# Kernel tuning notes

Measured on AMD Instinct MI355X. Metric: run time of the kernel, lower is better.

Reference implementation:

```python
import jax, jax.numpy as jnp
import numpy as np

B, T, HID = 4, 2048, 1024
H, D = 16, 64  # num_heads, depth = hidden // heads
NEG_INF = -1e9


def setup_inputs() -> dict:
    key = jax.random.key(0)
    ks = jax.random.split(key, 8)
    s = 1.0 / np.sqrt(HID)
    return {
        "q": jax.random.normal(ks[0], (B, T, HID), jnp.float32),
        "k": jax.random.normal(ks[1], (B, T, HID), jnp.float32),
        "v": jax.random.normal(ks[2], (B, T, HID), jnp.float32),
        "pad_mask": jax.random.randint(ks[3], (B, T), 0, 2, jnp.int32),
        "Wq": jax.random.normal(ks[4], (HID, HID), jnp.float32) * s,
        "Wk": jax.random.normal(ks[5], (HID, HID), jnp.float32) * s,
        "Wv": jax.random.normal(ks[6], (HID, HID), jnp.float32) * s,
        "Wo": jax.random.normal(ks[7], (HID, HID), jnp.float32) * s,
    }


def _split_heads(x):
    # [B, T, HID] -> [B*H, T, D]
    b, t, _ = x.shape
    return x.reshape(b, t, H, D).transpose(0, 2, 1, 3).reshape(b * H, t, D)


def _combine_heads(x):
    # [B*H, T, D] -> [B, T, HID]
    t = x.shape[1]
    return x.reshape(-1, H, t, D).transpose(0, 2, 1, 3).reshape(-1, t, HID)


def reference(q, k, v, pad_mask, Wq, Wk, Wv, Wo):
    qp = _split_heads(q @ Wq) * (D ** -0.5)   # [B*H, Tq, D]
    kp = _split_heads(k @ Wk)                  # [B*H, Tk, D]
    vp = _split_heads(v @ Wv)                  # [B*H, Tk, D]
    # additive pad bias: repeat([H,1]) is head-major tiling, reproduced via jnp.tile
    bias = jnp.tile(pad_mask.astype(jnp.float32) * NEG_INF, (H, 1))[:, None, :]
    logits = jnp.einsum('bqd,bkd->bqk', qp, kp) + bias  # [B*H, Tq, Tk]
    weights = jax.nn.softmax(logits, axis=-1)
    # original calls functional.dropout but discards the result -> no-op
    out = jnp.einsum('bqk,bkd->bqd', weights, vp)
    out = _combine_heads(out)                  # [B, Tq, HID]
    return out @ Wo
```

## Files before the change

kernel.cpp:

```cpp
#include <hip/hip_runtime.h>
#include <hip/hip_bf16.h>

#define TQ 2048
#define HIDDEN 1024
#define NB 4
#define NH 16
#define DH 64
#define BHN (NB*NH)
#define LOG2E 1.44269504f

typedef __attribute__((ext_vector_type(4))) float f32x4;
typedef __attribute__((ext_vector_type(8))) short s16x8;

#if __has_builtin(__builtin_amdgcn_exp2f)
#define EXP2(x) __builtin_amdgcn_exp2f(x)
#else
#define EXP2(x) exp2f(x)
#endif

__device__ inline unsigned short f2bf(float f) {
    union { float f; unsigned int u; } x; x.f = f;
    unsigned int r = x.u + 0x7fffu + ((x.u >> 16) & 1u);
    return (unsigned short)(r >> 16);
}

__device__ inline unsigned int pkbf(float a, float b) {
    __hip_bfloat162 h = __float22bfloat162_rn(make_float2(a, b));
    return *reinterpret_cast<unsigned int*>(&h);
}

union PBU { uint4 u4; s16x8 v; };

#define GLL16(gsrc, ldst) \
    __builtin_amdgcn_global_load_lds( \
        (const __attribute__((address_space(1))) unsigned int*)(gsrc), \
        (__attribute__((address_space(3))) unsigned int*)(ldst), 16, 0, 0)

__global__ __launch_bounds__(256) void maskprep(const int* __restrict__ pad,
                                                unsigned short* __restrict__ maskAndB) {
    int p = blockIdx.x * 256 + threadIdx.x;
    int r = p >> 11, off = p & 2047;
    int o6 = off & 63;
    int ks = o6 >> 5, k32 = o6 & 31;
    int lg = k32 >> 3, j = k32 & 7;
    int key = (off & ~63) | (ks * 32 + ((j >> 2) << 4) + (lg << 2) + (j & 3));
    maskAndB[p] = pad[r * 2048 + key] ? (unsigned short)0 : (unsigned short)0xFFFF;
}

__global__ __launch_bounds__(256) void wt_kernel(const float* W0, const float* W1,
                                                 const float* W2, const float* W3,
                                                 unsigned short* Wt) {
    const float* W = (blockIdx.z == 0) ? W0 : (blockIdx.z == 1) ? W1
                    : (blockIdx.z == 2) ? W2 : W3;
    unsigned short* out = Wt + (size_t)blockIdx.z * HIDDEN * HIDDEN;
    __shared__ float tile[64][68];
    int t = threadIdx.x;
    int k0 = blockIdx.y * 64, n0 = blockIdx.x * 64;
#pragma unroll
    for (int i = 0; i < 4; i++) {
        int r = (t >> 4) + i * 16;
        int c = (t & 15) * 4;
        float4 v = *(const float4*)(W + (size_t)(k0 + r) * HIDDEN + n0 + c);
        tile[r][c] = v.x; tile[r][c+1] = v.y; tile[r][c+2] = v.z; tile[r][c+3] = v.w;
    }
    __syncthreads();
#pragma unroll
    for (int i = 0; i < 4; i++) {
        int n = (t >> 4) + i * 16;
        int kc = (t & 15) * 4;
        ushort4 o;
        o.x = f2bf(tile[kc+0][n]); o.y = f2bf(tile[kc+1][n]);
        o.z = f2bf(tile[kc+2][n]); o.w = f2bf(tile[kc+3][n]);
        *(ushort4*)(out + (size_t)(n0 + n) * HIDDEN + k0 + kc) = o;
    }
}

__global__ __launch_bounds__(256) void gemm_proj(const float* __restrict__ A,
                                                 const unsigned short* __restrict__ Bt,
                                                 unsigned short* __restrict__ outb,
                                                 float scale, int vt) {
    __shared__ alignas(16) float As[128 * 64];
    __shared__ alignas(16) unsigned short Bs[128 * 64];
    const int t = threadIdx.x;
    const int wave = t >> 6, lane = t & 63;
    const int wr = wave >> 1, wc = wave & 1;
    const int lr = lane & 15, lg = lane >> 4;
    const int linear = blockIdx.x + 8 * blockIdx.y;
    const int tile = ((linear & 7) << 6) | (linear >> 3);
    const int m0 = (tile >> 3) * 128, n0 = (tile & 7) * 128;

    size_t gA[8];
#pragma unroll
    for (int i = 0; i < 8; i++) {
        int f = i * 256 + t;
        int row = f >> 4, sg = (f & 15) ^ (row & 15);
        gA[i] = (size_t)(m0 + row) * HIDDEN + sg * 4;
    }
    size_t gB[4];
#pragma unroll
    for (int i = 0; i < 4; i++) {
        int f = i * 256 + t;
        int row = f >> 3, sg = (f & 7) ^ (row & 7);
        gB[i] = (size_t)(n0 + row) * HIDDEN + sg * 8;
    }

    f32x4 acc[4][4] = {};

    for (int k0 = 0; k0 < HIDDEN; k0 += 64) {
        __syncthreads();
#pragma unroll
        for (int i = 0; i < 8; i++)
            GLL16(A + gA[i] + k0, &As[(size_t)(i * 256 + wave * 64) * 4]);
#pragma unroll
        for (int i = 0; i < 4; i++)
            GLL16(Bt + gB[i] + k0, &Bs[(size_t)(i * 256 + wave * 64) * 8]);
        __syncthreads();
#pragma unroll
        for (int q = 0; q < 2; q++) {
            s16x8 af[4], bfr[4];
#pragma unroll
            for (int mi = 0; mi < 4; mi++) {
                int row = wr * 64 + mi * 16 + lr;
                int s0 = (q * 8 + lg * 2) ^ (row & 15);
                int s1 = (q * 8 + lg * 2 + 1) ^ (row & 15);
                float4 a0 = *(const float4*)(&As[row * 64 + s0 * 4]);
                float4 a1 = *(const float4*)(&As[row * 64 + s1 * 4]);
                PBU u;
                u.u4.x = pkbf(a0.x, a0.y); u.u4.y = pkbf(a0.z, a0.w);
                u.u4.z = pkbf(a1.x, a1.y); u.u4.w = pkbf(a1.z, a1.w);
                af[mi] = u.v;
            }
#pragma unroll
            for (int ni = 0; ni < 4; ni++) {
                int row = wc * 64 + ni * 16 + lr;
                int s = (q * 4 + lg) ^ (row & 7);
                bfr[ni] = *(const s16x8*)(&Bs[row * 64 + s * 8]);
            }
#pragma unroll
            for (int mi = 0; mi < 4; mi++)
#pragma unroll
                for (int ni = 0; ni < 4; ni++)
                    acc[mi][ni] = __builtin_amdgcn_mfma_f32_16x16x32_bf16(af[mi], bfr[ni], acc[mi][ni], 0, 0, 0);
        }
    }

    if (vt == 0) {
#pragma unroll
        for (int mi = 0; mi < 4; mi++)
#pragma unroll
            for (int ni = 0; ni < 4; ni++)
#pragma unroll
                for (int j = 0; j < 4; j++) {
                    int m = m0 + wr * 64 + mi * 16 + lg * 4 + j;
                    int n = n0 + wc * 64 + ni * 16 + lr;
                    int b = m >> 11, tt = m & (TQ - 1);
                    int h = n >> 6, d = n & 63;
                    outb[((size_t)(b * NH + h) * TQ + tt) * DH + d] = f2bf(acc[mi][ni][j] * scale);
                }
    } else {
#pragma unroll
        for (int mi = 0; mi < 4; mi++)
#pragma unroll
            for (int ni = 0; ni < 4; ni++) {
                int m = m0 + wr * 64 + mi * 16 + lg * 4;
                int n = n0 + wc * 64 + ni * 16 + lr;
                int b = m >> 11, tt = m & (TQ - 1);
                int h = n >> 6, d = n & 63;
                ushort4 pk;
                pk.x = f2bf(acc[mi][ni][0] * scale);
                pk.y = f2bf(acc[mi][ni][1] * scale);
                pk.z = f2bf(acc[mi][ni][2] * scale);
                pk.w = f2bf(acc[mi][ni][3] * scale);
                *(ushort4*)(outb + ((size_t)(b * NH + h) * DH + d) * TQ + tt) = pk;
            }
    }
}

__global__ __launch_bounds__(256) void gemm_out(const unsigned short* __restrict__ A,
                                                const unsigned short* __restrict__ Bt,
                                                float* __restrict__ out) {
    __shared__ alignas(16) unsigned short As[128 * 64];
    __shared__ alignas(16) unsigned short Bs[128 * 64];
    const int t = threadIdx.x;
    const int wave = t >> 6, lane = t & 63;
    const int wr = wave >> 1, wc = wave & 1;
    const int lr = lane & 15, lg = lane >> 4;
    const int linear = blockIdx.x + 8 * blockIdx.y;
    const int tile = ((linear & 7) << 6) | (linear >> 3);
    const int m0 = (tile >> 3) * 128, n0 = (tile & 7) * 128;

    size_t gA[4], gB[4];
#pragma unroll
    for (int i = 0; i < 4; i++) {
        int f = i * 256 + t;
        int row = f >> 3, sg = (f & 7) ^ (row & 7);
        gA[i] = (size_t)(m0 + row) * HIDDEN + sg * 8;
        gB[i] = (size_t)(n0 + row) * HIDDEN + sg * 8;
    }

    f32x4 acc[4][4] = {};

    for (int k0 = 0; k0 < HIDDEN; k0 += 64) {
        __syncthreads();
#pragma unroll
        for (int i = 0; i < 4; i++) {
            GLL16(A + gA[i] + k0, &As[(size_t)(i * 256 + wave * 64) * 8]);
            GLL16(Bt + gB[i] + k0, &Bs[(size_t)(i * 256 + wave * 64) * 8]);
        }
        __syncthreads();
#pragma unroll
        for (int q = 0; q < 2; q++) {
            s16x8 af[4], bfr[4];
#pragma unroll
            for (int mi = 0; mi < 4; mi++) {
                int row = wr * 64 + mi * 16 + lr;
                int s = (q * 4 + lg) ^ (row & 7);
                af[mi] = *(const s16x8*)(&As[row * 64 + s * 8]);
            }
#pragma unroll
            for (int ni = 0; ni < 4; ni++) {
                int row = wc * 64 + ni * 16 + lr;
                int s = (q * 4 + lg) ^ (row & 7);
                bfr[ni] = *(const s16x8*)(&Bs[row * 64 + s * 8]);
            }
#pragma unroll
            for (int mi = 0; mi < 4; mi++)
#pragma unroll
                for (int ni = 0; ni < 4; ni++)
                    acc[mi][ni] = __builtin_amdgcn_mfma_f32_16x16x32_bf16(af[mi], bfr[ni], acc[mi][ni], 0, 0, 0);
        }
    }
#pragma unroll
    for (int mi = 0; mi < 4; mi++)
#pragma unroll
        for (int ni = 0; ni < 4; ni++)
#pragma unroll
            for (int j = 0; j < 4; j++) {
                int m = m0 + wr * 64 + mi * 16 + lg * 4 + j;
                int n = n0 + wc * 64 + ni * 16 + lr;
                out[(size_t)m * HIDDEN + n] = acc[mi][ni][j];
            }
}

__global__ __launch_bounds__(512, 4) void attn_kernel(
        const unsigned short* __restrict__ QP,
        const unsigned short* __restrict__ KP,
        const unsigned short* __restrict__ VT,
        const unsigned short* __restrict__ maskAndB,
        unsigned short* __restrict__ AO) {
    __shared__ alignas(16) unsigned short Ks[2][64 * 72];
    __shared__ alignas(16) unsigned short Vs[2][64 * 72];
    const int t = threadIdx.x, wave = t >> 6, lane = t & 63;
    const int lr = lane & 15, lg = lane >> 4;
    const int linear = blockIdx.x + 8 * blockIdx.y;
    const int bh = ((linear & 7) << 3) | ((linear >> 3) & 7);
    const int qb = linear >> 6;
    const int q0 = qb * 256 + wave * 32;
    const unsigned short* Qb = QP + (size_t)bh * TQ * DH;
    const unsigned short* Kb = KP + (size_t)bh * TQ * DH;
    const unsigned short* Vb = VT + (size_t)bh * DH * TQ;
    const unsigned short* mrow = maskAndB + (bh & (NB - 1)) * TQ;

    const short ob = (short)0x3F80;
    const s16x8 ones = {ob, ob, ob, ob, ob, ob, ob, ob};

    s16x8 qf[2][2];
#pragma unroll
    for (int u = 0; u < 2; u++)
#pragma unroll
        for (int h = 0; h < 2; h++)
            qf[u][h] = *(const s16x8*)(Qb + (size_t)(q0 + u * 16 + lr) * DH + h * 32 + lg * 8);

    const int srow = t >> 3, scol = (t & 7) * 8;
    const unsigned short* kA = Kb + srow * DH + scol;
    const unsigned short* vA = Vb + (size_t)srow * TQ + scol;
    const int ksO = srow * 72 + scol;
    const int cc = t & 7;
    const int vg = ((cc & 4) << 1) + ((cc & 1) << 2) + ((cc >> 1) & 1);
    const int vO = srow * 72 + vg * 4;

    uint4 kr, vr;
#define LOAD_TILE(kt_) do { \
        kr = *(const uint4*)(kA + (size_t)(kt_) * 4096); \
        vr = *(const uint4*)(vA + (size_t)(kt_) * 64); \
    } while (0)
#define STORE_TILE(b_) do { \
        *(uint4*)(&Ks[b_][ksO]) = kr; \
        *(uint2*)(&Vs[b_][vO])     = make_uint2(vr.x, vr.y); \
        *(uint2*)(&Vs[b_][vO + 8]) = make_uint2(vr.z, vr.w); \
    } while (0)

    f32x4 o[2][4] = {};
    f32x4 osum[2] = {};

    LOAD_TILE(0);
    STORE_TILE(0);

    const int NT = TQ / 64;
    for (int kt = 0; kt < NT; kt++) {
        __syncthreads();
        const int cur = kt & 1;
        if (kt + 1 < NT) LOAD_TILE(kt + 1);
        uint4 ma0 = *(const uint4*)(mrow + kt * 64 + lg * 8);
        uint4 ma1 = *(const uint4*)(mrow + kt * 64 + 32 + lg * 8);

        f32x4 z[2][4] = {};
#pragma unroll
        for (int ni = 0; ni < 4; ni++) {
            s16x8 kf0 = *(const s16x8*)(&Ks[cur][(ni * 16 + lr) * 72 + lg * 8]);
            s16x8 kf1 = *(const s16x8*)(&Ks[cur][(ni * 16 + lr) * 72 + 32 + lg * 8]);
#pragma unroll
            for (int u = 0; u < 2; u++) {
                z[u][ni] = __builtin_amdgcn_mfma_f32_16x16x32_bf16(kf0, qf[u][0], z[u][ni], 0, 0, 0);
                z[u][ni] = __builtin_amdgcn_mfma_f32_16x16x32_bf16(kf1, qf[u][1], z[u][ni], 0, 0, 0);
            }
        }

        PBU pb[2][2];
#pragma unroll
        for (int u = 0; u < 2; u++) {
#pragma unroll
            for (int ni = 0; ni < 4; ni++)
#pragma unroll
                for (int r = 0; r < 4; r++)
                    z[u][ni][r] = EXP2(z[u][ni][r]);
#pragma unroll
            for (int ks = 0; ks < 2; ks++) {
                pb[u][ks].u4.x = pkbf(z[u][2 * ks][0], z[u][2 * ks][1]);
                pb[u][ks].u4.y = pkbf(z[u][2 * ks][2], z[u][2 * ks][3]);
                pb[u][ks].u4.z = pkbf(z[u][2 * ks + 1][0], z[u][2 * ks + 1][1]);
                pb[u][ks].u4.w = pkbf(z[u][2 * ks + 1][2], z[u][2 * ks + 1][3]);
            }
            pb[u][0].u4.x &= ma0.x; pb[u][0].u4.y &= ma0.y;
            pb[u][0].u4.z &= ma0.z; pb[u][0].u4.w &= ma0.w;
            pb[u][1].u4.x &= ma1.x; pb[u][1].u4.y &= ma1.y;
            pb[u][1].u4.z &= ma1.z; pb[u][1].u4.w &= ma1.w;
        }

#pragma unroll
        for (int di = 0; di < 4; di++)
#pragma unroll
            for (int ks = 0; ks < 2; ks++) {
                s16x8 vf = *(const s16x8*)(&Vs[cur][(di * 16 + lr) * 72 + ks * 32 + lg * 8]);
#pragma unroll
                for (int u = 0; u < 2; u++)
                    o[u][di] = __builtin_amdgcn_mfma_f32_16x16x32_bf16(vf, pb[u][ks].v, o[u][di], 0, 0, 0);
            }
#pragma unroll
        for (int u = 0; u < 2; u++) {
            osum[u] = __builtin_amdgcn_mfma_f32_16x16x32_bf16(ones, pb[u][0].v, osum[u], 0, 0, 0);
            osum[u] = __builtin_amdgcn_mfma_f32_16x16x32_bf16(ones, pb[u][1].v, osum[u], 0, 0, 0);
        }

        if (kt + 1 < NT) STORE_TILE((kt + 1) & 1);
    }

    const int b = bh >> 4, h = bh & 15;
#pragma unroll
    for (int u = 0; u < 2; u++) {
        float inv = 1.f / osum[u][0];
        int tt = q0 + u * 16 + lr;
#pragma unroll
        for (int di = 0; di < 4; di++) {
            uint2 w;
            w.x = pkbf(o[u][di][0] * inv, o[u][di][1] * inv);
            w.y = pkbf(o[u][di][2] * inv, o[u][di][3] * inv);
            *(uint2*)(AO + (size_t)(b * TQ + tt) * HIDDEN + h * 64 + di * 16 + lg * 4) = w;
        }
    }
#undef LOAD_TILE
#undef STORE_TILE
}

extern "C" void kernel_launch(void* const* d_in, const int* in_sizes, int n_in,
                              void* d_out, int out_size, void* d_ws, size_t ws_size,
                              hipStream_t stream) {
    const float* q  = (const float*)d_in[0];
    const float* k  = (const float*)d_in[1];
    const float* v  = (const float*)d_in[2];
    const int* pad  = (const int*)d_in[3];
    const float* Wq = (const float*)d_in[4];
    const float* Wk = (const float*)d_in[5];
    const float* Wv = (const float*)d_in[6];
    const float* Wo = (const float*)d_in[7];
    float* out = (float*)d_out;

    unsigned short* ws = (unsigned short*)d_ws;
    unsigned short* Wt = ws;
    unsigned short* AO = ws + (size_t)4 * 1024 * 1024;
    unsigned short* QP = AO + (size_t)BHN * TQ * DH;
    unsigned short* KP = QP + (size_t)BHN * TQ * DH;
    unsigned short* VTb = KP + (size_t)BHN * TQ * DH;
    unsigned short* maskAndB = VTb + (size_t)BHN * TQ * DH;
    (void)ws_size; (void)in_sizes; (void)n_in; (void)out_size;

    dim3 b256(256);
    const dim3 gGemm(8, 64);
    maskprep<<<dim3(NB * TQ / 256), b256, 0, stream>>>(pad, maskAndB);
    wt_kernel<<<dim3(16, 16, 4), b256, 0, stream>>>(Wq, Wk, Wv, Wo, Wt);
    gemm_proj<<<gGemm, b256, 0, stream>>>(q, Wt + (size_t)0 * 1024 * 1024, QP, 0.125f * LOG2E, 0);
    gemm_proj<<<gGemm, b256, 0, stream>>>(k, Wt + (size_t)1 * 1024 * 1024, KP, 1.0f, 0);
    gemm_proj<<<gGemm, b256, 0, stream>>>(v, Wt + (size_t)2 * 1024 * 1024, VTb, 1.0f, 1);
    attn_kernel<<<dim3(8, 64), dim3(512), 0, stream>>>(QP, KP, VTb, maskAndB, AO);
    gemm_out<<<gGemm, b256, 0, stream>>>(AO, Wt + (size_t)3 * 1024 * 1024, out);
}
```

Before: 203.8 us.

## Use 1024-thread attention blocks with 16 query rows per wave

The attention kernel moves from 512 threads with 32 query rows per wave to 1024 threads with 16 rows per wave. The K/V tile loads are split so the first half of the threads loads K and the second half loads V. This is meant to raise wave-level parallelism and cut per-wave register use. In exchange, each K/V tile read from LDS is reused by fewer query rows per wave, so LDS traffic per MFMA rises, and the larger block raises barrier cost.

New measurement: 213.4 us. +4.7%, slower.

```diff
diff --git a/kernel.cpp b/kernel.cpp
--- a/kernel.cpp
+++ b/kernel.cpp
@@ -242,7 +242,7 @@
             }
 }
 
-__global__ __launch_bounds__(512, 4) void attn_kernel(
+__global__ __launch_bounds__(1024, 8) void attn_kernel(
         const unsigned short* __restrict__ QP,
         const unsigned short* __restrict__ KP,
         const unsigned short* __restrict__ VT,
@@ -255,7 +255,7 @@
     const int linear = blockIdx.x + 8 * blockIdx.y;
     const int bh = ((linear & 7) << 3) | ((linear >> 3) & 7);
     const int qb = linear >> 6;
-    const int q0 = qb * 256 + wave * 32;
+    const int q0 = qb * 256 + wave * 16;
     const unsigned short* Qb = QP + (size_t)bh * TQ * DH;
     const unsigned short* Kb = KP + (size_t)bh * TQ * DH;
     const unsigned short* Vb = VT + (size_t)bh * DH * TQ;
@@ -264,34 +264,35 @@
     const short ob = (short)0x3F80;
     const s16x8 ones = {ob, ob, ob, ob, ob, ob, ob, ob};
 
-    s16x8 qf[2][2];
-#pragma unroll
-    for (int u = 0; u < 2; u++)
-#pragma unroll
-        for (int h = 0; h < 2; h++)
-            qf[u][h] = *(const s16x8*)(Qb + (size_t)(q0 + u * 16 + lr) * DH + h * 32 + lg * 8);
-
-    const int srow = t >> 3, scol = (t & 7) * 8;
+    s16x8 qf0 = *(const s16x8*)(Qb + (size_t)(q0 + lr) * DH + lg * 8);
+    s16x8 qf1 = *(const s16x8*)(Qb + (size_t)(q0 + lr) * DH + 32 + lg * 8);
+
+    const int st = t & 511;
+    const int srow = st >> 3, scol = (st & 7) * 8;
+    const bool isK = t < 512;
     const unsigned short* kA = Kb + srow * DH + scol;
     const unsigned short* vA = Vb + (size_t)srow * TQ + scol;
     const int ksO = srow * 72 + scol;
-    const int cc = t & 7;
+    const int cc = st & 7;
     const int vg = ((cc & 4) << 1) + ((cc & 1) << 2) + ((cc >> 1) & 1);
     const int vO = srow * 72 + vg * 4;
 
-    uint4 kr, vr;
+    uint4 r;
 #define LOAD_TILE(kt_) do { \
-        kr = *(const uint4*)(kA + (size_t)(kt_) * 4096); \
-        vr = *(const uint4*)(vA + (size_t)(kt_) * 64); \
+        r = isK ? *(const uint4*)(kA + (size_t)(kt_) * 4096) \
+                : *(const uint4*)(vA + (size_t)(kt_) * 64); \
     } while (0)
 #define STORE_TILE(b_) do { \
-        *(uint4*)(&Ks[b_][ksO]) = kr; \
-        *(uint2*)(&Vs[b_][vO])     = make_uint2(vr.x, vr.y); \
-        *(uint2*)(&Vs[b_][vO + 8]) = make_uint2(vr.z, vr.w); \
+        if (isK) { \
+            *(uint4*)(&Ks[b_][ksO]) = r; \
+        } else { \
+            *(uint2*)(&Vs[b_][vO])     = make_uint2(r.x, r.y); \
+            *(uint2*)(&Vs[b_][vO + 8]) = make_uint2(r.z, r.w); \
+        } \
     } while (0)
 
-    f32x4 o[2][4] = {};
-    f32x4 osum[2] = {};
+    f32x4 o[4] = {};
+    f32x4 osum = {};
 
     LOAD_TILE(0);
     STORE_TILE(0);
@@ -304,69 +305,55 @@
         uint4 ma0 = *(const uint4*)(mrow + kt * 64 + lg * 8);
         uint4 ma1 = *(const uint4*)(mrow + kt * 64 + 32 + lg * 8);
 
-        f32x4 z[2][4] = {};
+        f32x4 z[4] = {};
 #pragma unroll
         for (int ni = 0; ni < 4; ni++) {
             s16x8 kf0 = *(const s16x8*)(&Ks[cur][(ni * 16 + lr) * 72 + lg * 8]);
             s16x8 kf1 = *(const s16x8*)(&Ks[cur][(ni * 16 + lr) * 72 + 32 + lg * 8]);
-#pragma unroll
-            for (int u = 0; u < 2; u++) {
-                z[u][ni] = __builtin_amdgcn_mfma_f32_16x16x32_bf16(kf0, qf[u][0], z[u][ni], 0, 0, 0);
-                z[u][ni] = __builtin_amdgcn_mfma_f32_16x16x32_bf16(kf1, qf[u][1], z[u][ni], 0, 0, 0);
-            }
-        }
-
-        PBU pb[2][2];
-#pragma unroll
-        for (int u = 0; u < 2; u++) {
-#pragma unroll
-            for (int ni = 0; ni < 4; ni++)
-#pragma unroll
-                for (int r = 0; r < 4; r++)
-                    z[u][ni][r] = EXP2(z[u][ni][r]);
-#pragma unroll
-            for (int ks = 0; ks < 2; ks++) {
-                pb[u][ks].u4.x = pkbf(z[u][2 * ks][0], z[u][2 * ks][1]);
-                pb[u][ks].u4.y = pkbf(z[u][2 * ks][2], z[u][2 * ks][3]);
-                pb[u][ks].u4.z = pkbf(z[u][2 * ks + 1][0], z[u][2 * ks + 1][1]);
-                pb[u][ks].u4.w = pkbf(z[u][2 * ks + 1][2], z[u][2 * ks + 1][3]);
-            }
-            pb[u][0].u4.x &= ma0.x; pb[u][0].u4.y &= ma0.y;
-            pb[u][0].u4.z &= ma0.z; pb[u][0].u4.w &= ma0.w;
-            pb[u][1].u4.x &= ma1.x; pb[u][1].u4.y &= ma1.y;
-            pb[u][1].u4.z &= ma1.z; pb[u][1].u4.w &= ma1.w;
-        }
+            z[ni] = __builtin_amdgcn_mfma_f32_16x16x32_bf16(kf0, qf0, z[ni], 0, 0, 0);
+            z[ni] = __builtin_amdgcn_mfma_f32_16x16x32_bf16(kf1, qf1, z[ni], 0, 0, 0);
+        }
+
+#pragma unroll
+        for (int ni = 0; ni < 4; ni++)
+#pragma unroll
+            for (int rr = 0; rr < 4; rr++)
+                z[ni][rr] = EXP2(z[ni][rr]);
+        PBU pb[2];
+#pragma unroll
+        for (int ks = 0; ks < 2; ks++) {
+            pb[ks].u4.x = pkbf(z[2 * ks][0], z[2 * ks][1]);
+            pb[ks].u4.y = pkbf(z[2 * ks][2], z[2 * ks][3]);
+            pb[ks].u4.z = pkbf(z[2 * ks + 1][0], z[2 * ks + 1][1]);
+            pb[ks].u4.w = pkbf(z[2 * ks + 1][2], z[2 * ks + 1][3]);
+        }
+        pb[0].u4.x &= ma0.x; pb[0].u4.y &= ma0.y;
+        pb[0].u4.z &= ma0.z; pb[0].u4.w &= ma0.w;
+        pb[1].u4.x &= ma1.x; pb[1].u4.y &= ma1.y;
+        pb[1].u4.z &= ma1.z; pb[1].u4.w &= ma1.w;
 
 #pragma unroll
         for (int di = 0; di < 4; di++)
 #pragma unroll
             for (int ks = 0; ks < 2; ks++) {
                 s16x8 vf = *(const s16x8*)(&Vs[cur][(di * 16 + lr) * 72 + ks * 32 + lg * 8]);
-#pragma unroll
-                for (int u = 0; u < 2; u++)
-                    o[u][di] = __builtin_amdgcn_mfma_f32_16x16x32_bf16(vf, pb[u][ks].v, o[u][di], 0, 0, 0);
-            }
-#pragma unroll
-        for (int u = 0; u < 2; u++) {
-            osum[u] = __builtin_amdgcn_mfma_f32_16x16x32_bf16(ones, pb[u][0].v, osum[u], 0, 0, 0);
-            osum[u] = __builtin_amdgcn_mfma_f32_16x16x32_bf16(ones, pb[u][1].v, osum[u], 0, 0, 0);
-        }
+                o[di] = __builtin_amdgcn_mfma_f32_16x16x32_bf16(vf, pb[ks].v, o[di], 0, 0, 0);
+            }
+        osum = __builtin_amdgcn_mfma_f32_16x16x32_bf16(ones, pb[0].v, osum, 0, 0, 0);
+        osum = __builtin_amdgcn_mfma_f32_16x16x32_bf16(ones, pb[1].v, osum, 0, 0, 0);
 
         if (kt + 1 < NT) STORE_TILE((kt + 1) & 1);
     }
 
     const int b = bh >> 4, h = bh & 15;
-#pragma unroll
-    for (int u = 0; u < 2; u++) {
-        float inv = 1.f / osum[u][0];
-        int tt = q0 + u * 16 + lr;
-#pragma unroll
-        for (int di = 0; di < 4; di++) {
-            uint2 w;
-            w.x = pkbf(o[u][di][0] * inv, o[u][di][1] * inv);
-            w.y = pkbf(o[u][di][2] * inv, o[u][di][3] * inv);
-            *(uint2*)(AO + (size_t)(b * TQ + tt) * HIDDEN + h * 64 + di * 16 + lg * 4) = w;
-        }
+    float inv = 1.f / osum[0];
+    int tt = q0 + lr;
+#pragma unroll
+    for (int di = 0; di < 4; di++) {
+        uint2 w;
+        w.x = pkbf(o[di][0] * inv, o[di][1] * inv);
+        w.y = pkbf(o[di][2] * inv, o[di][3] * inv);
+        *(uint2*)(AO + (size_t)(b * TQ + tt) * HIDDEN + h * 64 + di * 16 + lg * 4) = w;
     }
 #undef LOAD_TILE
 #undef STORE_TILE
@@ -401,6 +388,6 @@
     gemm_proj<<<gGemm, b256, 0, stream>>>(q, Wt + (size_t)0 * 1024 * 1024, QP, 0.125f * LOG2E, 0);
     gemm_proj<<<gGemm, b256, 0, stream>>>(k, Wt + (size_t)1 * 1024 * 1024, KP, 1.0f, 0);
     gemm_proj<<<gGemm, b256, 0, stream>>>(v, Wt + (size_t)2 * 1024 * 1024, VTb, 1.0f, 1);
-    attn_kernel<<<dim3(8, 64), dim3(512), 0, stream>>>(QP, KP, VTb, maskAndB, AO);
+    attn_kernel<<<dim3(8, 64), dim3(1024), 0, stream>>>(QP, KP, VTb, maskAndB, AO);
     gemm_out<<<gGemm, b256, 0, stream>>>(AO, Wt + (size_t)3 * 1024 * 1024, out);
 }
```
